# Optimization experiments

Hardware: AMD Instinct MI355X
Metric: run time of the kernel (lower is better)

The kernel has to match this reference:

```python
import jax, jax.numpy as jnp
import numpy as np
from jax import lax

VOCAB = 35095 + 2
WORD_DIM = 300
MAX_SENT = 3000
N_FILT = 100
N_CLASSES = 10


def setup_inputs() -> dict:
    key = jax.random.key(0)
    ks = jax.random.split(key, 10)
    x = jax.random.randint(ks[0], (2, MAX_SENT), 0, VOCAB)
    emb = jax.random.normal(ks[1], (VOCAB, WORD_DIM), dtype=jnp.float32) * 0.1
    emb = emb.at[0].set(0.0)  # padding_idx=0
    w1 = jax.random.normal(ks[2], (N_FILT, 1, 3), dtype=jnp.float32) * 0.1
    b1 = jax.random.normal(ks[3], (N_FILT,), dtype=jnp.float32) * 0.01
    w2 = jax.random.normal(ks[4], (N_FILT, 1, 4), dtype=jnp.float32) * 0.1
    b2 = jax.random.normal(ks[5], (N_FILT,), dtype=jnp.float32) * 0.01
    w3 = jax.random.normal(ks[6], (N_FILT, 1, 5), dtype=jnp.float32) * 0.1
    b3 = jax.random.normal(ks[7], (N_FILT,), dtype=jnp.float32) * 0.01
    fc_w = jax.random.normal(ks[8], (N_CLASSES, 3 * N_FILT), dtype=jnp.float32) * 0.05
    fc_b = jax.random.normal(ks[9], (N_CLASSES,), dtype=jnp.float32) * 0.01
    return {"x": x, "emb": emb, "w1": w1, "b1": b1, "w2": w2, "b2": b2,
            "w3": w3, "b3": b3, "fc_w": fc_w, "fc_b": fc_b}


def _conv_relu_maxpool(h, w, b):
    # h: [B, 1, L]; w: [F, 1, K]  ->  [B, F]
    y = lax.conv_general_dilated(h, w, window_strides=(1,), padding='VALID',
                                 dimension_numbers=('NCW', 'OIW', 'NCW'))
    y = jnp.maximum(y + b[None, :, None], 0.0)
    return jnp.max(y, axis=2)


def reference(x, emb, w1, b1, w2, b2, w3, b3, fc_w, fc_b):
    # Embedding lookup then flatten to a single-channel 1D signal of length 900k
    h = emb[x].reshape(-1, 1, WORD_DIM * MAX_SENT)  # [B, 1, 900000]
    c1 = _conv_relu_maxpool(h, w1, b1)  # [B, 100]
    c2 = _conv_relu_maxpool(h, w2, b2)
    c3 = _conv_relu_maxpool(h, w3, b3)
    feats = jnp.concatenate([c1, c2, c3], axis=1)  # [B, 300]
    # Dropout is identity at inference
    return feats @ fc_w.T + fc_b
```

## Files before the change

### kernel.cpp

```cpp
#include <hip/hip_runtime.h>

#define VOCAB   35097
#define DDIM    300
#define NWORDS  3000
#define L_SIG   900000
#define NFILT   100
#define NCLS    10

#define QQ      28
#define HALF    14
#define WIN     (QQ + 4)
#define NHP     (HALF + 4)
#define BLK_POS (64 * QQ)
#define NBLKA   503
#define FPG     5
#define NGRPW   5

typedef __attribute__((ext_vector_type(2))) float f32x2;

__device__ __forceinline__ float relu_(float v) { return fmaxf(v, 0.0f); }

__device__ __forceinline__ f32x2 pk_mul(f32x2 a, f32x2 b) {
  f32x2 d;
  asm("v_pk_mul_f32 %0, %1, %2" : "=v"(d) : "v"(a), "v"(b));
  return d;
}
__device__ __forceinline__ f32x2 pk_fma(f32x2 a, f32x2 b, f32x2 c) {
  f32x2 d;
  asm("v_pk_fma_f32 %0, %1, %2, %3" : "=v"(d) : "v"(a), "v"(b), "v"(c));
  return d;
}
__device__ __forceinline__ f32x2 dup2(float w) { f32x2 d; d.x = w; d.y = w; return d; }

template<bool TAIL>
__device__ __forceinline__ void run_group(
    const float (&h)[WIN], const f32x2 (&hp)[NHP], int t0, int f0, int lane,
    const float* __restrict__ w1, const float* __restrict__ w2,
    const float* __restrict__ w3,
    float* __restrict__ pslot)
{
  int n3 = QQ, n4 = QQ, n5 = QQ;
  if (TAIL) {
    n3 = min(max(899998 - t0, 0), QQ);
    n4 = min(max(899997 - t0, 0), QQ);
    n5 = min(max(899996 - t0, 0), QQ);
  }
  const float NEG = -__builtin_huge_valf();

  float a3[FPG], a4[FPG], a5[FPG];

  #pragma unroll
  for (int j = 0; j < FPG; ++j) {
    const int fu = __builtin_amdgcn_readfirstlane(f0 + j);
    const float a0 = w1[fu*3+0], a1 = w1[fu*3+1], a2 = w1[fu*3+2];
    const float c0 = w2[fu*4+0], c1 = w2[fu*4+1], c2 = w2[fu*4+2], c3 = w2[fu*4+3];
    const float e0 = w3[fu*5+0], e1 = w3[fu*5+1], e2 = w3[fu*5+2], e3 = w3[fu*5+3], e4 = w3[fu*5+4];

    float m3a = NEG, m3b = NEG, m4a = NEG, m4b = NEG, m5a = NEG, m5b = NEG;

    if (!TAIL) {
      const f32x2 pa0 = dup2(a0), pa1 = dup2(a1), pa2 = dup2(a2);
      const f32x2 pc0 = dup2(c0), pc1 = dup2(c1), pc2 = dup2(c2), pc3 = dup2(c3);
      const f32x2 pe0 = dup2(e0), pe1 = dup2(e1), pe2 = dup2(e2), pe3 = dup2(e3), pe4 = dup2(e4);

      #pragma unroll
      for (int p = 0; p < HALF; ++p) {
        f32x2 t3 = pk_mul(pa2, hp[p+2]);
        t3 = pk_fma(pa1, hp[p+1], t3);
        t3 = pk_fma(pa0, hp[p+0], t3);
        f32x2 t4 = pk_mul(pc3, hp[p+3]);
        t4 = pk_fma(pc2, hp[p+2], t4);
        t4 = pk_fma(pc1, hp[p+1], t4);
        t4 = pk_fma(pc0, hp[p+0], t4);
        f32x2 t5 = pk_mul(pe4, hp[p+4]);
        t5 = pk_fma(pe3, hp[p+3], t5);
        t5 = pk_fma(pe2, hp[p+2], t5);
        t5 = pk_fma(pe1, hp[p+1], t5);
        t5 = pk_fma(pe0, hp[p+0], t5);
        if (p & 1) {
          m3b = fmaxf(fmaxf(m3b, t3.x), t3.y);
          m4b = fmaxf(fmaxf(m4b, t4.x), t4.y);
          m5b = fmaxf(fmaxf(m5b, t5.x), t5.y);
        } else {
          m3a = fmaxf(fmaxf(m3a, t3.x), t3.y);
          m4a = fmaxf(fmaxf(m4a, t4.x), t4.y);
          m5a = fmaxf(fmaxf(m5a, t5.x), t5.y);
        }
      }
    } else {
      #pragma unroll
      for (int p = 0; p < QQ; ++p) {
        float v3 = fmaf(a0, h[p], fmaf(a1, h[p+1], a2 * h[p+2]));
        float v4 = fmaf(c0, h[p], fmaf(c1, h[p+1], fmaf(c2, h[p+2], c3 * h[p+3])));
        float v5 = fmaf(e0, h[p], fmaf(e1, h[p+1], fmaf(e2, h[p+2], fmaf(e3, h[p+3], e4 * h[p+4]))));
        if (p < n3) { if (p & 1) m3b = fmaxf(m3b, v3); else m3a = fmaxf(m3a, v3); }
        if (p < n4) { if (p & 1) m4b = fmaxf(m4b, v4); else m4a = fmaxf(m4a, v4); }
        if (p < n5) { if (p & 1) m5b = fmaxf(m5b, v5); else m5a = fmaxf(m5a, v5); }
      }
    }
    a3[j] = fmaxf(m3a, m3b);
    a4[j] = fmaxf(m4a, m4b);
    a5[j] = fmaxf(m5a, m5b);
  }

  #pragma unroll
  for (int s = 1; s < 64; s <<= 1) {
    #pragma unroll
    for (int j = 0; j < FPG; ++j) {
      a3[j] = fmaxf(a3[j], __shfl_xor(a3[j], s));
      a4[j] = fmaxf(a4[j], __shfl_xor(a4[j], s));
      a5[j] = fmaxf(a5[j], __shfl_xor(a5[j], s));
    }
  }

  if (lane == 0) {
    #pragma unroll
    for (int j = 0; j < FPG; ++j) {
      pslot[j]      = a3[j];
      pslot[5 + j]  = a4[j];
      pslot[10 + j] = a5[j];
    }
  }
}

__global__ __launch_bounds__(256, 4) void conv_max_kernel(
    const int* __restrict__ x, const float* __restrict__ emb,
    const float* __restrict__ w1, const float* __restrict__ w2,
    const float* __restrict__ w3,
    float* __restrict__ partial)
{
  const int lane  = threadIdx.x & 63;
  const int wave  = threadIdx.x >> 6;
  const int batch = blockIdx.y;
  const int t0_blk = blockIdx.x * BLK_POS;
  const int t0     = t0_blk + lane * QQ;
  const int fbase  = wave * (FPG * NGRPW);

  float h[WIN];
  {
    int w0 = t0 / DDIM;
    int d0 = t0 - w0 * DDIM;
    int wa = min(w0, NWORDS - 1);
    int wb = min(w0 + 1, NWORDS - 1);
    int xa = x[batch * NWORDS + wa];
    int xb = x[batch * NWORDS + wb];
    const float4* rowA = (const float4*)(emb + (size_t)xa * DDIM) + (d0 >> 2);
    const float4* rowB = (const float4*)(emb + (size_t)xb * DDIM);
    const int nf4 = (DDIM - d0) >> 2;
    #pragma unroll
    for (int i = 0; i < WIN / 4; ++i) {
      const float4* src = (i < nf4) ? (rowA + i) : (rowB + (i - nf4));
      float4 v = *src;
      h[4*i+0] = v.x; h[4*i+1] = v.y; h[4*i+2] = v.z; h[4*i+3] = v.w;
    }
  }

  f32x2 hp[NHP];
  #pragma unroll
  for (int k = 0; k < NHP; ++k) { f32x2 t; t.x = h[k]; t.y = h[k + HALF]; hp[k] = t; }

  float* pwave = partial + ((size_t)batch * NBLKA + blockIdx.x) * 300 + wave * 75;

  const bool tail = (t0_blk + BLK_POS + 4) > L_SIG;
  if (tail) {
    #pragma unroll 1
    for (int g = 0; g < NGRPW; ++g)
      run_group<true >(h, hp, t0, fbase + g * FPG, lane, w1, w2, w3, pwave + g * 15);
  } else {
    #pragma unroll 1
    for (int g = 0; g < NGRPW; ++g)
      run_group<false>(h, hp, t0, fbase + g * FPG, lane, w1, w2, w3, pwave + g * 15);
  }
}

__global__ __launch_bounds__(320) void reduce_kernel(
    const float* __restrict__ partial,
    const float* __restrict__ b1,
    const float* __restrict__ b2,
    const float* __restrict__ b3,
    float* __restrict__ feats)
{
  const int b = blockIdx.x;
  const int p = threadIdx.x;
  if (p >= 300) return;

  const float* col = partial + (size_t)b * NBLKA * 300 + p;
  float m = -__builtin_huge_valf();
  int i = 0;
  for (; i + 8 <= NBLKA; i += 8) {
    float v0 = col[(size_t)(i+0) * 300];
    float v1 = col[(size_t)(i+1) * 300];
    float v2 = col[(size_t)(i+2) * 300];
    float v3 = col[(size_t)(i+3) * 300];
    float v4 = col[(size_t)(i+4) * 300];
    float v5 = col[(size_t)(i+5) * 300];
    float v6 = col[(size_t)(i+6) * 300];
    float v7 = col[(size_t)(i+7) * 300];
    m = fmaxf(fmaxf(m, v0), v1);
    m = fmaxf(fmaxf(m, v2), v3);
    m = fmaxf(fmaxf(m, v4), v5);
    m = fmaxf(fmaxf(m, v6), v7);
  }
  for (; i < NBLKA; ++i)
    m = fmaxf(m, col[(size_t)i * 300]);

  const int wv = p / 75, r = p % 75, g = r / 15, q = r % 15;
  const int conv = q / 5, j = q % 5;
  const int f = wv * 25 + g * 5 + j;
  const float bias = (conv == 0) ? b1[f] : (conv == 1) ? b2[f] : b3[f];
  feats[b * 300 + conv * NFILT + f] = relu_(m + bias);
}

__global__ void fc_kernel(const float* __restrict__ feats,
                          const float* __restrict__ fcw,
                          const float* __restrict__ fcb,
                          float* __restrict__ out)
{
  const int b = blockIdx.x / NCLS;
  const int c = blockIdx.x % NCLS;
  const int lane = threadIdx.x;
  float s = 0.0f;
  for (int k = lane; k < 3 * NFILT; k += 64)
    s += feats[b * 3 * NFILT + k] * fcw[c * 3 * NFILT + k];
  #pragma unroll
  for (int k = 1; k < 64; k <<= 1) s += __shfl_xor(s, k);
  if (lane == 0) out[b * NCLS + c] = s + fcb[c];
}

extern "C" void kernel_launch(void* const* d_in, const int* in_sizes, int n_in,
                              void* d_out, int out_size, void* d_ws, size_t ws_size,
                              hipStream_t stream)
{
  const int*   x   = (const int*)  d_in[0];
  const float* emb = (const float*)d_in[1];
  const float* w1  = (const float*)d_in[2];
  const float* b1  = (const float*)d_in[3];
  const float* w2  = (const float*)d_in[4];
  const float* b2  = (const float*)d_in[5];
  const float* w3  = (const float*)d_in[6];
  const float* b3  = (const float*)d_in[7];
  const float* fcw = (const float*)d_in[8];
  const float* fcb = (const float*)d_in[9];
  float* out = (float*)d_out;

  float* partial = (float*)d_ws;
  float* feats   = partial + (size_t)2 * NBLKA * 300;

  dim3 grid(NBLKA, 2);
  conv_max_kernel<<<grid, 256, 0, stream>>>(x, emb, w1, w2, w3, partial);
  reduce_kernel<<<2, 320, 0, stream>>>(partial, b1, b2, b3, feats);
  fc_kernel<<<2 * NCLS, 64, 0, stream>>>(feats, fcw, fcb, out);
}
```

Before: 183.7 us.

## Fuse conv, reduction and FC into one kernel using last-block atomic counter

Merges the three launches into a single kernel. Each block now handles two sub-tiles with 512 threads, and the last block to finish, found through an atomic counter and threadfence, does the cross-block max reduction in chunks through shared memory, then the bias, ReLU and the FC layer. This removes two kernel launches and their gaps. In exchange it adds a memset launch, an atomic per block and a serial tail reduction done by one block. It also uses a larger block size with launch_bounds(512,4), which may pressure registers.

```diff
diff --git a/kernel.cpp b/kernel.cpp
--- a/kernel.cpp
+++ b/kernel.cpp
@@ -8,13 +8,16 @@
 #define NCLS    10
 
 #define QQ      28
-#define HALF    14
+#define HALFQ   14
 #define WIN     (QQ + 4)
-#define NHP     (HALF + 4)
-#define BLK_POS (64 * QQ)
-#define NBLKA   503
+#define NHP     (HALFQ + 4)
+#define SUBPOS  (64 * QQ)
+#define NBX     252
+#define ROWS    (NBX * 2)
 #define FPG     5
 #define NGRPW   5
+#define NCHK    8
+#define CHKR    (ROWS / NCHK)
 
 typedef __attribute__((ext_vector_type(2))) float f32x2;
 
@@ -64,7 +67,7 @@
       const f32x2 pe0 = dup2(e0), pe1 = dup2(e1), pe2 = dup2(e2), pe3 = dup2(e3), pe4 = dup2(e4);
 
       #pragma unroll
-      for (int p = 0; p < HALF; ++p) {
+      for (int p = 0; p < HALFQ; ++p) {
         f32x2 t3 = pk_mul(pa2, hp[p+2]);
         t3 = pk_fma(pa1, hp[p+1], t3);
         t3 = pk_fma(pa0, hp[p+0], t3);
@@ -123,18 +126,26 @@
   }
 }
 
-__global__ __launch_bounds__(256, 4) void conv_max_kernel(
+__global__ __launch_bounds__(512, 4) void cnn_fused_kernel(
     const int* __restrict__ x, const float* __restrict__ emb,
-    const float* __restrict__ w1, const float* __restrict__ w2,
-    const float* __restrict__ w3,
-    float* __restrict__ partial)
+    const float* __restrict__ w1, const float* __restrict__ b1,
+    const float* __restrict__ w2, const float* __restrict__ b2,
+    const float* __restrict__ w3, const float* __restrict__ b3,
+    const float* __restrict__ fcw, const float* __restrict__ fcb,
+    float* __restrict__ partial,
+    unsigned int* __restrict__ counter,
+    float* __restrict__ out)
 {
-  const int lane  = threadIdx.x & 63;
-  const int wave  = threadIdx.x >> 6;
+  const int tid   = threadIdx.x;
+  const int lane  = tid & 63;
+  const int wave  = tid >> 6;
+  const int w4    = wave & 3;
+  const int half  = wave >> 2;
   const int batch = blockIdx.y;
-  const int t0_blk = blockIdx.x * BLK_POS;
-  const int t0     = t0_blk + lane * QQ;
-  const int fbase  = wave * (FPG * NGRPW);
+  const int row   = blockIdx.x * 2 + half;
+  const int sub0  = blockIdx.x * (2 * SUBPOS) + half * SUBPOS;
+  const int t0    = sub0 + lane * QQ;
+  const int fbase = w4 * (FPG * NGRPW);
 
   float h[WIN];
   {
@@ -157,11 +168,11 @@
 
   f32x2 hp[NHP];
   #pragma unroll
-  for (int k = 0; k < NHP; ++k) { f32x2 t; t.x = h[k]; t.y = h[k + HALF]; hp[k] = t; }
-
-  float* pwave = partial + ((size_t)batch * NBLKA + blockIdx.x) * 300 + wave * 75;
-
-  const bool tail = (t0_blk + BLK_POS + 4) > L_SIG;
+  for (int k = 0; k < NHP; ++k) { f32x2 t; t.x = h[k]; t.y = h[k + HALFQ]; hp[k] = t; }
+
+  float* pwave = partial + ((size_t)batch * ROWS + row) * 300 + w4 * 75;
+
+  const bool tail = (sub0 + SUBPOS + 4) > L_SIG;
   if (tail) {
     #pragma unroll 1
     for (int g = 0; g < NGRPW; ++g)
@@ -171,60 +182,69 @@
     for (int g = 0; g < NGRPW; ++g)
       run_group<false>(h, hp, t0, fbase + g * FPG, lane, w1, w2, w3, pwave + g * 15);
   }
-}
-
-__global__ __launch_bounds__(320) void reduce_kernel(
-    const float* __restrict__ partial,
-    const float* __restrict__ b1,
-    const float* __restrict__ b2,
-    const float* __restrict__ b3,
-    float* __restrict__ feats)
-{
-  const int b = blockIdx.x;
-  const int p = threadIdx.x;
-  if (p >= 300) return;
-
-  const float* col = partial + (size_t)b * NBLKA * 300 + p;
-  float m = -__builtin_huge_valf();
-  int i = 0;
-  for (; i + 8 <= NBLKA; i += 8) {
-    float v0 = col[(size_t)(i+0) * 300];
-    float v1 = col[(size_t)(i+1) * 300];
-    float v2 = col[(size_t)(i+2) * 300];
-    float v3 = col[(size_t)(i+3) * 300];
-    float v4 = col[(size_t)(i+4) * 300];
-    float v5 = col[(size_t)(i+5) * 300];
-    float v6 = col[(size_t)(i+6) * 300];
-    float v7 = col[(size_t)(i+7) * 300];
-    m = fmaxf(fmaxf(m, v0), v1);
-    m = fmaxf(fmaxf(m, v2), v3);
-    m = fmaxf(fmaxf(m, v4), v5);
-    m = fmaxf(fmaxf(m, v6), v7);
-  }
-  for (; i < NBLKA; ++i)
-    m = fmaxf(m, col[(size_t)i * 300]);
-
-  const int wv = p / 75, r = p % 75, g = r / 15, q = r % 15;
-  const int conv = q / 5, j = q % 5;
-  const int f = wv * 25 + g * 5 + j;
-  const float bias = (conv == 0) ? b1[f] : (conv == 1) ? b2[f] : b3[f];
-  feats[b * 300 + conv * NFILT + f] = relu_(m + bias);
-}
-
-__global__ void fc_kernel(const float* __restrict__ feats,
-                          const float* __restrict__ fcw,
-                          const float* __restrict__ fcb,
-                          float* __restrict__ out)
-{
-  const int b = blockIdx.x / NCLS;
-  const int c = blockIdx.x % NCLS;
-  const int lane = threadIdx.x;
-  float s = 0.0f;
-  for (int k = lane; k < 3 * NFILT; k += 64)
-    s += feats[b * 3 * NFILT + k] * fcw[c * 3 * NFILT + k];
-  #pragma unroll
-  for (int k = 1; k < 64; k <<= 1) s += __shfl_xor(s, k);
-  if (lane == 0) out[b * NCLS + c] = s + fcb[c];
+
+  __shared__ int s_last;
+  __threadfence();
+  __syncthreads();
+  if (tid == 0) {
+    unsigned int old = atomicAdd(counter, 1u);
+    s_last = (old == (unsigned int)(NBX * 2 - 1));
+  }
+  __syncthreads();
+  if (!s_last) return;
+  __threadfence();
+
+  __shared__ float4 chunkres[150][NCHK];
+  __shared__ float  s_feats[2][3 * NFILT];
+
+  for (int task = tid; task < 2 * 75 * NCHK; task += 512) {
+    const int chunk = task / 150;
+    const int rem   = task % 150;
+    const int bi    = rem / 75;
+    const int c4    = rem % 75;
+    const float* base = partial + ((size_t)bi * ROWS + chunk * CHKR) * 300 + c4 * 4;
+    float4 m; m.x = m.y = m.z = m.w = -__builtin_huge_valf();
+    #pragma unroll 9
+    for (int r = 0; r < CHKR; ++r) {
+      float4 v = *(const float4*)(base + (size_t)r * 300);
+      m.x = fmaxf(m.x, v.x); m.y = fmaxf(m.y, v.y);
+      m.z = fmaxf(m.z, v.z); m.w = fmaxf(m.w, v.w);
+    }
+    chunkres[rem][chunk] = m;
+  }
+  __syncthreads();
+
+  if (tid < 150) {
+    float4 m = chunkres[tid][0];
+    #pragma unroll
+    for (int k = 1; k < NCHK; ++k) {
+      float4 v = chunkres[tid][k];
+      m.x = fmaxf(m.x, v.x); m.y = fmaxf(m.y, v.y);
+      m.z = fmaxf(m.z, v.z); m.w = fmaxf(m.w, v.w);
+    }
+    const int bi = tid / 75, c4 = tid % 75;
+    #pragma unroll
+    for (int e = 0; e < 4; ++e) {
+      const float ve = (e == 0) ? m.x : (e == 1) ? m.y : (e == 2) ? m.z : m.w;
+      const int p = c4 * 4 + e;
+      const int pw = p / 75, r2 = p % 75, g = r2 / 15, q = r2 % 15;
+      const int conv = q / 5, j = q % 5;
+      const int f = pw * 25 + g * 5 + j;
+      const float bias = (conv == 0) ? b1[f] : (conv == 1) ? b2[f] : b3[f];
+      s_feats[bi][conv * NFILT + f] = relu_(ve + bias);
+    }
+  }
+  __syncthreads();
+
+  for (int o = wave; o < 2 * NCLS; o += 8) {
+    const int ob = o / NCLS, oc = o % NCLS;
+    float s = 0.0f;
+    for (int k = lane; k < 3 * NFILT; k += 64)
+      s += s_feats[ob][k] * fcw[oc * 3 * NFILT + k];
+    #pragma unroll
+    for (int sft = 1; sft < 64; sft <<= 1) s += __shfl_xor(s, sft);
+    if (lane == 0) out[ob * NCLS + oc] = s + fcb[oc];
+  }
 }
 
 extern "C" void kernel_launch(void* const* d_in, const int* in_sizes, int n_in,
@@ -244,10 +264,11 @@
   float* out = (float*)d_out;
 
   float* partial = (float*)d_ws;
-  float* feats   = partial + (size_t)2 * NBLKA * 300;
-
-  dim3 grid(NBLKA, 2);
-  conv_max_kernel<<<grid, 256, 0, stream>>>(x, emb, w1, w2, w3, partial);
-  reduce_kernel<<<2, 320, 0, stream>>>(partial, b1, b2, b3, feats);
-  fc_kernel<<<2 * NCLS, 64, 0, stream>>>(feats, fcw, fcb, out);
-}
+  unsigned int* counter = (unsigned int*)(partial + (size_t)2 * ROWS * 300);
+
+  hipMemsetAsync(counter, 0, sizeof(unsigned int), stream);
+
+  dim3 grid(NBX, 2);
+  cnn_fused_kernel<<<grid, 512, 0, stream>>>(x, emb, w1, b1, w2, b2, w3, b3,
+                                             fcw, fcb, partial, counter, out);
+}
```

Result: slower. 220.2 us (+19.9%).
